# Kernel tuning notes

Measured on AMD Instinct MI355X. Metric: run time of the kernel, lower is better.

## Reference

```python
import jax, jax.numpy as jnp
import numpy as np

EMBED = 768
HEADS = 32
HEAD_DIM = EMBED // HEADS  # 24
T = 512
B = 16


def setup_inputs() -> dict:
    key = jax.random.key(0)
    ks = jax.random.split(key, 10)
    s = 1.0 / np.sqrt(EMBED)
    inp = {
        "query": jax.random.normal(ks[0], (T, B, EMBED), dtype=jnp.float32),
        "attn_bias": jax.random.normal(ks[1], (B * HEADS, T, T), dtype=jnp.float32),
        "Wq": jax.random.normal(ks[2], (EMBED, EMBED), dtype=jnp.float32) * s,
        "bq": jnp.zeros((EMBED,), dtype=jnp.float32),
        "Wk": jax.random.normal(ks[3], (EMBED, EMBED), dtype=jnp.float32) * s,
        "bk": jnp.zeros((EMBED,), dtype=jnp.float32),
        "Wv": jax.random.normal(ks[4], (EMBED, EMBED), dtype=jnp.float32) * s,
        "bv": jnp.zeros((EMBED,), dtype=jnp.float32),
        "Wo": jax.random.normal(ks[5], (EMBED, EMBED), dtype=jnp.float32) * s,
        "bo": jnp.zeros((EMBED,), dtype=jnp.float32),
    }
    return inp


def _split_heads(x):
    # [T, B, E] -> [B, H, T, d]
    t, b, _ = x.shape
    return x.reshape(t, b, HEADS, HEAD_DIM).transpose(1, 2, 0, 3)


def reference(query, attn_bias, Wq, bq, Wk, bk, Wv, bv, Wo, bo):
    t, b, e = query.shape
    scaling = HEAD_DIM ** (-0.5)
    # projections (torch Linear: x @ W.T + b)
    q = (query @ Wq.T + bq) * scaling
    k = query @ Wk.T + bk
    v = query @ Wv.T + bv
    qh, kh, vh = _split_heads(q), _split_heads(k), _split_heads(v)  # [B,H,T,d]
    scores = jnp.einsum('bhtd,bhsd->bhts', qh, kh)
    scores = scores + attn_bias.reshape(b, HEADS, t, t)
    probs = jax.nn.softmax(scores, axis=-1)  # dropout = identity (eval)
    attn = jnp.einsum('bhts,bhsd->bhtd', probs, vh)  # [B,H,T,d]
    attn = attn.transpose(2, 0, 1, 3).reshape(t, b, e)  # [T,B,E]
    out = attn @ Wo.T + bo  # final dropout = identity (eval)
    return out
```

## Files before the change

kernel.cpp:

```cpp
#include <hip/hip_runtime.h>
#include <hip/hip_bf16.h>

#define T_SEQ 512
#define BATCH 16
#define EMB 768
#define HEADS 32
#define HDIM 24
#define ROWS (T_SEQ * BATCH)
#define SCALING 0.20412414523193154f

__global__ __launch_bounds__(256)
void qkv_proj_kernel(const float* __restrict__ X,
                     const float* __restrict__ Wq, const float* __restrict__ Wk,
                     const float* __restrict__ Wv,
                     const float* __restrict__ bq, const float* __restrict__ bk,
                     const float* __restrict__ bv,
                     float* __restrict__ qo, float* __restrict__ ko,
                     float* __restrict__ vo)
{
    __shared__ __attribute__((aligned(16))) float Xs[16][132];
    __shared__ __attribute__((aligned(16))) float Ws[16][132];

    const int tid = threadIdx.x;
    const int r0 = blockIdx.x * 128;
    const int nb = blockIdx.y;
    const int which = nb / 6;
    const int n0 = (nb % 6) * 128;
    const float* W    = (which == 0) ? Wq : (which == 1) ? Wk : Wv;
    const float* bias = (which == 0) ? bq : (which == 1) ? bk : bv;
    float* out        = (which == 0) ? qo : (which == 1) ? ko : vo;

    const int tx = tid & 15;
    const int ty = tid >> 4;

    const int srow = tid >> 2;
    const int skq  = (tid & 3) << 2;

    float acc[8][8] = {};

    for (int k0 = 0; k0 < EMB; k0 += 16) {
        const float4 x0 = *(const float4*)(X + (size_t)(r0 + srow) * EMB + k0 + skq);
        const float4 x1 = *(const float4*)(X + (size_t)(r0 + srow + 64) * EMB + k0 + skq);
        const float4 w0 = *(const float4*)(W + (size_t)(n0 + srow) * EMB + k0 + skq);
        const float4 w1 = *(const float4*)(W + (size_t)(n0 + srow + 64) * EMB + k0 + skq);
        __syncthreads();
        Xs[skq + 0][srow] = x0.x; Xs[skq + 1][srow] = x0.y;
        Xs[skq + 2][srow] = x0.z; Xs[skq + 3][srow] = x0.w;
        Xs[skq + 0][srow + 64] = x1.x; Xs[skq + 1][srow + 64] = x1.y;
        Xs[skq + 2][srow + 64] = x1.z; Xs[skq + 3][srow + 64] = x1.w;
        Ws[skq + 0][srow] = w0.x; Ws[skq + 1][srow] = w0.y;
        Ws[skq + 2][srow] = w0.z; Ws[skq + 3][srow] = w0.w;
        Ws[skq + 0][srow + 64] = w1.x; Ws[skq + 1][srow + 64] = w1.y;
        Ws[skq + 2][srow + 64] = w1.z; Ws[skq + 3][srow + 64] = w1.w;
        __syncthreads();
#pragma unroll
        for (int kk = 0; kk < 16; ++kk) {
            const float4 a0 = *(const float4*)&Xs[kk][ty * 4];
            const float4 a1 = *(const float4*)&Xs[kk][ty * 4 + 64];
            const float4 b0 = *(const float4*)&Ws[kk][tx * 4];
            const float4 b1 = *(const float4*)&Ws[kk][tx * 4 + 64];
            const float a[8] = {a0.x, a0.y, a0.z, a0.w, a1.x, a1.y, a1.z, a1.w};
            const float b[8] = {b0.x, b0.y, b0.z, b0.w, b1.x, b1.y, b1.z, b1.w};
#pragma unroll
            for (int ii = 0; ii < 8; ++ii)
#pragma unroll
                for (int jj = 0; jj < 8; ++jj)
                    acc[ii][jj] += a[ii] * b[jj];
        }
    }

#pragma unroll
    for (int im = 0; im < 2; ++im)
#pragma unroll
    for (int ii = 0; ii < 4; ++ii) {
        const int rr = r0 + im * 64 + ty * 4 + ii;
        const int t = rr >> 4;
        const int b = rr & 15;
#pragma unroll
        for (int jn = 0; jn < 2; ++jn)
#pragma unroll
        for (int jj = 0; jj < 4; ++jj) {
            const int nn = n0 + jn * 64 + tx * 4 + jj;
            float c = acc[im * 4 + ii][jn * 4 + jj] + bias[nn];
            if (which == 0) c *= SCALING;
            const int h = nn / HDIM;
            const int dd = nn - h * HDIM;
            out[((size_t)((b * HEADS + h) * T_SEQ + t)) * HDIM + dd] = c;
        }
    }
}

__global__ __launch_bounds__(256)
void attn_kernel(const float* __restrict__ qb, const float* __restrict__ kb,
                 const float* __restrict__ vb, const float* __restrict__ bias,
                 float* __restrict__ attn)
{
    const int bh = blockIdx.x;
    const int t0 = blockIdx.y * 16;
    const int tid = threadIdx.x;

    __shared__ float Ss[16][513];
    __shared__ float red[16][17];
    __shared__ float rowm[16];
    __shared__ float rowl[16];

    const float* Kb = kb + (size_t)bh * T_SEQ * HDIM;
    const float* Vb = vb + (size_t)bh * T_SEQ * HDIM;
    const float* Bb = bias + (size_t)bh * T_SEQ * T_SEQ + (size_t)t0 * T_SEQ;

    const int i = tid >> 4;
    const int g = tid & 15;

    float q[HDIM];
    {
        const float* qr = qb + ((size_t)bh * T_SEQ + t0 + i) * HDIM;
#pragma unroll
        for (int dd = 0; dd < HDIM; ++dd) q[dd] = qr[dd];
    }

    for (int s = g; s < T_SEQ; s += 16) {
        const float* kr = Kb + s * HDIM;
        float d = 0.f;
#pragma unroll
        for (int dd = 0; dd < HDIM; ++dd) d += q[dd] * kr[dd];
        Ss[i][s] = d + Bb[i * T_SEQ + s];
    }
    __syncthreads();

    float m = -1e30f;
    for (int s = g; s < T_SEQ; s += 16) m = fmaxf(m, Ss[i][s]);
    red[i][g] = m;
    __syncthreads();
    if (g == 0) {
        float mm = red[i][0];
#pragma unroll
        for (int j = 1; j < 16; ++j) mm = fmaxf(mm, red[i][j]);
        rowm[i] = mm;
    }
    __syncthreads();
    const float mrow = rowm[i];
    float l = 0.f;
    for (int s = g; s < T_SEQ; s += 16) {
        const float p = __expf(Ss[i][s] - mrow);
        Ss[i][s] = p;
        l += p;
    }
    red[i][g] = l;
    __syncthreads();
    if (g == 0) {
        float ll = 0.f;
#pragma unroll
        for (int j = 0; j < 16; ++j) ll += red[i][j];
        rowl[i] = 1.f / ll;
    }
    __syncthreads();

    for (int p = tid; p < 16 * HDIM; p += 256) {
        const int ii = p / HDIM, dd = p - ii * HDIM;
        float accv = 0.f;
        const float* vp = Vb + dd;
#pragma unroll 8
        for (int s = 0; s < T_SEQ; ++s) accv += Ss[ii][s] * vp[s * HDIM];
        accv *= rowl[ii];
        const int t = t0 + ii;
        const int b = bh >> 5;
        const int h = bh & 31;
        attn[((size_t)(t * BATCH + b)) * EMB + h * HDIM + dd] = accv;
    }
}

__global__ __launch_bounds__(256)
void out_proj_kernel(const float* __restrict__ A, const float* __restrict__ Wo,
                     const float* __restrict__ bo, float* __restrict__ out)
{
    __shared__ __attribute__((aligned(16))) float Xs[16][132];
    __shared__ __attribute__((aligned(16))) float Ws[16][132];

    const int tid = threadIdx.x;
    const int r0 = blockIdx.x * 128;
    const int n0 = blockIdx.y * 128;

    const int tx = tid & 15;
    const int ty = tid >> 4;

    const int srow = tid >> 2;
    const int skq  = (tid & 3) << 2;

    float acc[8][8] = {};

    for (int k0 = 0; k0 < EMB; k0 += 16) {
        const float4 x0 = *(const float4*)(A + (size_t)(r0 + srow) * EMB + k0 + skq);
        const float4 x1 = *(const float4*)(A + (size_t)(r0 + srow + 64) * EMB + k0 + skq);
        const float4 w0 = *(const float4*)(Wo + (size_t)(n0 + srow) * EMB + k0 + skq);
        const float4 w1 = *(const float4*)(Wo + (size_t)(n0 + srow + 64) * EMB + k0 + skq);
        __syncthreads();
        Xs[skq + 0][srow] = x0.x; Xs[skq + 1][srow] = x0.y;
        Xs[skq + 2][srow] = x0.z; Xs[skq + 3][srow] = x0.w;
        Xs[skq + 0][srow + 64] = x1.x; Xs[skq + 1][srow + 64] = x1.y;
        Xs[skq + 2][srow + 64] = x1.z; Xs[skq + 3][srow + 64] = x1.w;
        Ws[skq + 0][srow] = w0.x; Ws[skq + 1][srow] = w0.y;
        Ws[skq + 2][srow] = w0.z; Ws[skq + 3][srow] = w0.w;
        Ws[skq + 0][srow + 64] = w1.x; Ws[skq + 1][srow + 64] = w1.y;
        Ws[skq + 2][srow + 64] = w1.z; Ws[skq + 3][srow + 64] = w1.w;
        __syncthreads();
#pragma unroll
        for (int kk = 0; kk < 16; ++kk) {
            const float4 a0 = *(const float4*)&Xs[kk][ty * 4];
            const float4 a1 = *(const float4*)&Xs[kk][ty * 4 + 64];
            const float4 b0 = *(const float4*)&Ws[kk][tx * 4];
            const float4 b1 = *(const float4*)&Ws[kk][tx * 4 + 64];
            const float a[8] = {a0.x, a0.y, a0.z, a0.w, a1.x, a1.y, a1.z, a1.w};
            const float b[8] = {b0.x, b0.y, b0.z, b0.w, b1.x, b1.y, b1.z, b1.w};
#pragma unroll
            for (int ii = 0; ii < 8; ++ii)
#pragma unroll
                for (int jj = 0; jj < 8; ++jj)
                    acc[ii][jj] += a[ii] * b[jj];
        }
    }

    const float4 bo0 = *(const float4*)(bo + n0 + tx * 4);
    const float4 bo1 = *(const float4*)(bo + n0 + 64 + tx * 4);
#pragma unroll
    for (int im = 0; im < 2; ++im)
#pragma unroll
    for (int ii = 0; ii < 4; ++ii) {
        const int rr = r0 + im * 64 + ty * 4 + ii;
        float4 c0, c1;
        c0.x = acc[im * 4 + ii][0] + bo0.x; c0.y = acc[im * 4 + ii][1] + bo0.y;
        c0.z = acc[im * 4 + ii][2] + bo0.z; c0.w = acc[im * 4 + ii][3] + bo0.w;
        c1.x = acc[im * 4 + ii][4] + bo1.x; c1.y = acc[im * 4 + ii][5] + bo1.y;
        c1.z = acc[im * 4 + ii][6] + bo1.z; c1.w = acc[im * 4 + ii][7] + bo1.w;
        *(float4*)(out + (size_t)rr * EMB + n0 + tx * 4) = c0;
        *(float4*)(out + (size_t)rr * EMB + n0 + 64 + tx * 4) = c1;
    }
}

extern "C" void kernel_launch(void* const* d_in, const int* in_sizes, int n_in,
                              void* d_out, int out_size, void* d_ws, size_t ws_size,
                              hipStream_t stream)
{
    const float* query = (const float*)d_in[0];
    const float* abias = (const float*)d_in[1];
    const float* Wq = (const float*)d_in[2];
    const float* bq = (const float*)d_in[3];
    const float* Wk = (const float*)d_in[4];
    const float* bk = (const float*)d_in[5];
    const float* Wv = (const float*)d_in[6];
    const float* bv = (const float*)d_in[7];
    const float* Wo = (const float*)d_in[8];
    const float* bo = (const float*)d_in[9];
    float* out = (float*)d_out;

    float* ws = (float*)d_ws;
    const size_t QKV_ELEMS = (size_t)BATCH * HEADS * T_SEQ * HDIM;
    float* qb = ws;
    float* kb = ws + QKV_ELEMS;
    float* vb = ws + 2 * QKV_ELEMS;
    float* ab = ws + 3 * QKV_ELEMS;

    dim3 gA(ROWS / 128, 18);
    qkv_proj_kernel<<<gA, 256, 0, stream>>>(query, Wq, Wk, Wv, bq, bk, bv, qb, kb, vb);

    dim3 gB(BATCH * HEADS, T_SEQ / 16);
    attn_kernel<<<gB, 256, 0, stream>>>(qb, kb, vb, abias, ab);

    dim3 gC(ROWS / 128, EMB / 128);
    out_proj_kernel<<<gC, 256, 0, stream>>>(ab, Wo, bo, out);
}
```

Baseline: 2.262 ms.

## Keep attention scores in registers and remap blocks for XCD locality

The attention kernel now holds each thread's 32 scores in registers and does max and sum with wave shuffles instead of a shared score matrix and several barriers. Each thread accumulates a partial P·V over its own keys, and the partials are reduced through shared memory. Q, K, V and bias loads are vectorised as float4. The grid is flattened so that all query tiles of a head map to the same XCD, which should improve K/V L2 reuse, at the cost of more registers and a larger shared reduction buffer.

```diff
diff --git a/kernel.cpp b/kernel.cpp
--- a/kernel.cpp
+++ b/kernel.cpp
@@ -95,77 +95,102 @@
                  const float* __restrict__ vb, const float* __restrict__ bias,
                  float* __restrict__ attn)
 {
-    const int bh = blockIdx.x;
-    const int t0 = blockIdx.y * 16;
+    const int f = blockIdx.x;
+    const int xcd = f & 7;
+    const int r = f >> 3;
+    const int bh = xcd * 64 + (r >> 5);
+    const int t0 = (r & 31) * 16;
+
     const int tid = threadIdx.x;
-
-    __shared__ float Ss[16][513];
-    __shared__ float red[16][17];
-    __shared__ float rowm[16];
-    __shared__ float rowl[16];
+    const int i = tid >> 4;
+    const int g = tid & 15;
+
+    __shared__ float red[16 * 16 * 25];
+    __shared__ float rowinv[16];
 
     const float* Kb = kb + (size_t)bh * T_SEQ * HDIM;
     const float* Vb = vb + (size_t)bh * T_SEQ * HDIM;
-    const float* Bb = bias + (size_t)bh * T_SEQ * T_SEQ + (size_t)t0 * T_SEQ;
-
-    const int i = tid >> 4;
-    const int g = tid & 15;
+    const float* Bb = bias + (size_t)bh * T_SEQ * T_SEQ + (size_t)(t0 + i) * T_SEQ;
 
     float q[HDIM];
     {
-        const float* qr = qb + ((size_t)bh * T_SEQ + t0 + i) * HDIM;
-#pragma unroll
-        for (int dd = 0; dd < HDIM; ++dd) q[dd] = qr[dd];
-    }
-
-    for (int s = g; s < T_SEQ; s += 16) {
-        const float* kr = Kb + s * HDIM;
-        float d = 0.f;
-#pragma unroll
-        for (int dd = 0; dd < HDIM; ++dd) d += q[dd] * kr[dd];
-        Ss[i][s] = d + Bb[i * T_SEQ + s];
-    }
+        const float4* qr = (const float4*)(qb + ((size_t)bh * T_SEQ + t0 + i) * HDIM);
+#pragma unroll
+        for (int u = 0; u < 6; ++u) {
+            const float4 qv = qr[u];
+            q[u * 4 + 0] = qv.x; q[u * 4 + 1] = qv.y;
+            q[u * 4 + 2] = qv.z; q[u * 4 + 3] = qv.w;
+        }
+    }
+
+    float p[32];
+#pragma unroll
+    for (int c = 0; c < 8; ++c) {
+        const float4 b4 = *(const float4*)(Bb + c * 64 + g * 4);
+        const float bb[4] = {b4.x, b4.y, b4.z, b4.w};
+#pragma unroll
+        for (int j = 0; j < 4; ++j) {
+            const int s = c * 64 + g * 4 + j;
+            const float4* kr = (const float4*)(Kb + (size_t)s * HDIM);
+            const float4 k0 = kr[0], k1 = kr[1], k2 = kr[2];
+            const float4 k3 = kr[3], k4 = kr[4], k5 = kr[5];
+            float d0 = q[0]  * k0.x + q[1]  * k0.y + q[2]  * k0.z + q[3]  * k0.w;
+            float d1 = q[4]  * k1.x + q[5]  * k1.y + q[6]  * k1.z + q[7]  * k1.w;
+            float d2 = q[8]  * k2.x + q[9]  * k2.y + q[10] * k2.z + q[11] * k2.w;
+            float d3 = q[12] * k3.x + q[13] * k3.y + q[14] * k3.z + q[15] * k3.w;
+            d0 += q[16] * k4.x + q[17] * k4.y + q[18] * k4.z + q[19] * k4.w;
+            d1 += q[20] * k5.x + q[21] * k5.y + q[22] * k5.z + q[23] * k5.w;
+            p[c * 4 + j] = (d0 + d1) + (d2 + d3) + bb[j];
+        }
+    }
+
+    float m = p[0];
+#pragma unroll
+    for (int k = 1; k < 32; ++k) m = fmaxf(m, p[k]);
+#pragma unroll
+    for (int st = 1; st < 16; st <<= 1) m = fmaxf(m, __shfl_xor(m, st, 16));
+
+    float l = 0.f;
+#pragma unroll
+    for (int k = 0; k < 32; ++k) { p[k] = __expf(p[k] - m); l += p[k]; }
+#pragma unroll
+    for (int st = 1; st < 16; st <<= 1) l += __shfl_xor(l, st, 16);
+    if (g == 0) rowinv[i] = 1.f / l;
+
+    float acc[HDIM] = {};
+#pragma unroll
+    for (int c = 0; c < 8; ++c) {
+#pragma unroll
+        for (int j = 0; j < 4; ++j) {
+            const int s = c * 64 + g * 4 + j;
+            const float4* vr = (const float4*)(Vb + (size_t)s * HDIM);
+            const float pk = p[c * 4 + j];
+#pragma unroll
+            for (int u = 0; u < 6; ++u) {
+                const float4 v4 = vr[u];
+                acc[u * 4 + 0] += pk * v4.x;
+                acc[u * 4 + 1] += pk * v4.y;
+                acc[u * 4 + 2] += pk * v4.z;
+                acc[u * 4 + 3] += pk * v4.w;
+            }
+        }
+    }
+
+    float* myred = red + (i * 16 + g) * 25;
+#pragma unroll
+    for (int dd = 0; dd < HDIM; ++dd) myred[dd] = acc[dd];
     __syncthreads();
 
-    float m = -1e30f;
-    for (int s = g; s < T_SEQ; s += 16) m = fmaxf(m, Ss[i][s]);
-    red[i][g] = m;
-    __syncthreads();
-    if (g == 0) {
-        float mm = red[i][0];
-#pragma unroll
-        for (int j = 1; j < 16; ++j) mm = fmaxf(mm, red[i][j]);
-        rowm[i] = mm;
-    }
-    __syncthreads();
-    const float mrow = rowm[i];
-    float l = 0.f;
-    for (int s = g; s < T_SEQ; s += 16) {
-        const float p = __expf(Ss[i][s] - mrow);
-        Ss[i][s] = p;
-        l += p;
-    }
-    red[i][g] = l;
-    __syncthreads();
-    if (g == 0) {
-        float ll = 0.f;
-#pragma unroll
-        for (int j = 0; j < 16; ++j) ll += red[i][j];
-        rowl[i] = 1.f / ll;
-    }
-    __syncthreads();
-
-    for (int p = tid; p < 16 * HDIM; p += 256) {
-        const int ii = p / HDIM, dd = p - ii * HDIM;
-        float accv = 0.f;
-        const float* vp = Vb + dd;
-#pragma unroll 8
-        for (int s = 0; s < T_SEQ; ++s) accv += Ss[ii][s] * vp[s * HDIM];
-        accv *= rowl[ii];
+    const int b = bh >> 5;
+    const int h = bh & 31;
+    for (int pp = tid; pp < 16 * HDIM; pp += 256) {
+        const int ii = pp / HDIM, dd = pp - ii * HDIM;
+        float a = 0.f;
+#pragma unroll
+        for (int gg = 0; gg < 16; ++gg) a += red[(ii * 16 + gg) * 25 + dd];
+        a *= rowinv[ii];
         const int t = t0 + ii;
-        const int b = bh >> 5;
-        const int h = bh & 31;
-        attn[((size_t)(t * BATCH + b)) * EMB + h * HDIM + dd] = accv;
+        attn[((size_t)(t * BATCH + b)) * EMB + h * HDIM + dd] = a;
     }
 }
 
@@ -262,8 +287,7 @@
     dim3 gA(ROWS / 128, 18);
     qkv_proj_kernel<<<gA, 256, 0, stream>>>(query, Wq, Wk, Wv, bq, bk, bv, qb, kb, vb);
 
-    dim3 gB(BATCH * HEADS, T_SEQ / 16);
-    attn_kernel<<<gB, 256, 0, stream>>>(qb, kb, vb, abias, ab);
+    attn_kernel<<<dim3(BATCH * HEADS * (T_SEQ / 16)), 256, 0, stream>>>(qb, kb, vb, abias, ab);
 
     dim3 gC(ROWS / 128, EMB / 128);
     out_proj_kernel<<<gC, 256, 0, stream>>>(ab, Wo, bo, out);
```

After: 3.762 ms. 1.66x slower.
